# Optimization experiments

Measured on AMD Instinct MI355X. Metric: run time of the kernel, lower is better.

## Reference

```python
import jax, jax.numpy as jnp
import numpy as np

K = (0.3, 0.3, 0.4)   # args.args_k_0..2
EPS = 1e-8


def squash(v, axis=-1):
    norm = jnp.linalg.norm(v, axis=axis, keepdims=True)
    scale = norm ** 2 / (1.0 + norm ** 2) / (norm + EPS)
    return scale * v


def setup_inputs() -> dict:
    key = jax.random.key(0)
    kx, kw = jax.random.split(key)
    B, IN, DIN, OUT, DOUT = 128, 4608, 8, 10, 16
    x = jax.random.normal(kx, (B, IN, DIN), dtype=jnp.float32)
    weight = 0.1 * jax.random.normal(kw, (OUT, IN, DOUT, DIN), dtype=jnp.float32)
    return {"x": x, "weight": weight}


def reference(x, weight):
    # x: [B, I, Din], weight: [O, I, Dout, Din]
    # x_hat[b,o,i,d] = sum_k weight[o,i,d,k] * x[b,i,k]
    x_hat = jnp.einsum('oidk,bik->boid', weight, x)  # [B, O, I, Dout]
    x_hat_d = jax.lax.stop_gradient(x_hat)
    B, O, I, D = x_hat.shape
    b = jnp.zeros((B, O, I), dtype=x.dtype)
    feats = []
    for it in range(3):
        c = jax.nn.softmax(b, axis=1)[..., None]          # [B, O, I, 1], softmax over out caps
        if it == 2:
            out = squash(jnp.sum(c * x_hat, axis=-2, keepdims=True))      # [B, O, 1, D]
        else:
            out = squash(jnp.sum(c * x_hat_d, axis=-2, keepdims=True))    # [B, O, 1, D]
            b = b + jnp.sum(out * x_hat_d, axis=-1)                       # agreement update
        feats.append(out * K[it])
    # stack -> [3, B, O, 1, D]; squeeze caps-sum axis; sum over iterations
    outputs = jnp.sum(jnp.squeeze(jnp.stack(feats), axis=-2), axis=0)     # [B, O, D]
    return outputs.reshape(B, O, 4, 4)
```

## Files before the change

### kernel.cpp

```cpp
#include <hip/hip_runtime.h>

#define B_    128
#define I_    4608
#define O_    10
#define D_    16
#define NCHUNKS 2304
#define NIB   64
#define CPB   36
#define CHH   2560
#define PSET  20480

typedef _Float16 f16x2 __attribute__((ext_vector_type(2)));
typedef _Float16 f16x4 __attribute__((ext_vector_type(4)));
typedef _Float16 f16x8 __attribute__((ext_vector_type(8)));
typedef float    f32x4 __attribute__((ext_vector_type(4)));
typedef __fp16   pk16x2 __attribute__((ext_vector_type(2)));
typedef unsigned int uint2v __attribute__((ext_vector_type(2)));

__device__ __forceinline__ f16x4 pack4(float a, float b, float c, float d) {
    union { f16x4 v; pk16x2 p[2]; } u;
    u.p[0] = __builtin_amdgcn_cvt_pkrtz(a, b);
    u.p[1] = __builtin_amdgcn_cvt_pkrtz(c, d);
    return u.v;
}
__device__ __forceinline__ f16x2 splat_h2(float a) {
    union { f16x2 v; pk16x2 p; } u;
    u.p = __builtin_amdgcn_cvt_pkrtz(a, a);
    return u.v;
}

__global__ __launch_bounds__(256)
void prep_kernel(const float* __restrict__ w, _Float16* __restrict__ pw)
{
    __shared__ float wch[2560];
    const int c = blockIdx.x, t = threadIdx.x;
#pragma unroll
    for (int o = 0; o < O_; ++o)
        wch[o * 256 + t] = w[(long)o * (I_ * 128) + (long)c * 256 + t];
    __syncthreads();

    _Float16* dst = pw + (long)c * CHH;
#pragma unroll
    for (int kk = 0; kk < 3; ++kk) {
        const int sidx = t + kk * 256;
        if (sidx < 640) {
            const int hg   = sidx & 1;
            const int lane = (sidx >> 1) & 63;
            const int p    = sidx >> 7;
            const int r = lane & 15, g = lane >> 4;
            const int o = 2 * p + hg;
            const float4 gg = *(const float4*)&wch[o * 256 + (g & 1) * 128 + r * 8 + (g >> 1) * 4];
            *(f16x4*)(dst + (long)sidx * 4) = pack4(gg.x, gg.y, gg.z, gg.w);
        }
    }
}

template<int MODE>
__global__ __launch_bounds__(512, 4)
void pass_kernel(const float* __restrict__ x,
                 const _Float16* __restrict__ pw,
                 const float* __restrict__ v,
                 float* __restrict__ parts)
{
    __shared__ float red[4 * 2560];

    const int tid  = threadIdx.x;
    const int lane = tid & 63;
    const int wv   = tid >> 6;
    const int bl   = lane & 15;
    const int g    = lane >> 4;
    const int u    = blockIdx.x;
    const int xcd  = u & 7, s = u >> 3;
    const int ib   = xcd * 8 + (s & 7);
    const int bg   = s >> 3;
    const int c0   = ib * CPB;
    const int cend = c0 + CPB;
    const int iloc = g & 1, kq = g >> 1;
    const int b0   = bg * 16 + bl;

    f16x4 idf;
#pragma unroll
    for (int j = 0; j < 4; ++j) idf[j] = (_Float16)((bl == 4 * g + j) ? 1.f : 0.f);

    f16x4 vf[O_];
    if (MODE == 1) {
#pragma unroll
        for (int o = 0; o < O_; ++o) {
            const float4 vv = *(const float4*)(v + ((long)b0 * O_ + o) * D_ + g * 4);
            vf[o] = pack4(vv.x, vv.y, vv.z, vv.w);
        }
    }

    f32x4 S[O_];
#pragma unroll
    for (int o = 0; o < O_; ++o) S[o] = (f32x4)(0.f);

    const long lofs = (long)lane * 8;
    auto fragp = [&](int c, int p) {
        return (const f16x8*)(pw + (long)c * CHH + p * 512 + lofs);
    };
    auto xp = [&](int c) {
        return (const float4*)(x + ((long)b0 * I_ + 2 * c + iloc) * 8 + kq * 4);
    };

    int c = c0 + wv;
    f16x8 f1[5];
    float4 xqC, xqN;
#pragma unroll
    for (int p = 0; p < 5; ++p) f1[p] = *fragp(c, p);
    xqC = *xp(c);

#pragma unroll
    for (int t5 = 0; t5 < 5; ++t5) {
        const bool valid = (c < cend);
        int cn = c + 8; if (cn > NCHUNKS - 1) cn = NCHUNKS - 1;
        if (valid) {
            xqN = *xp(cn);

            float cs[O_];
            if (MODE == 1) {
#pragma unroll
                for (int p = 0; p < 5; ++p) {
                    f16x4 pe, po;
                    pe[0]=f1[p][0]; pe[1]=f1[p][1]; pe[2]=f1[p][2]; pe[3]=f1[p][3];
                    po[0]=f1[p][4]; po[1]=f1[p][5]; po[2]=f1[p][6]; po[3]=f1[p][7];
                    const f32x4 te = __builtin_amdgcn_mfma_f32_16x16x16f16(pe, idf, (f32x4)(0.f), 0, 0, 0);
                    const f32x4 to = __builtin_amdgcn_mfma_f32_16x16x16f16(po, idf, (f32x4)(0.f), 0, 0, 0);
                    const f16x4 ae = pack4(te[0], te[1], te[2], te[3]);
                    const f16x4 ao = pack4(to[0], to[1], to[2], to[3]);
                    const f32x4 ua = __builtin_amdgcn_mfma_f32_16x16x16f16(ae, vf[2*p],   (f32x4)(0.f), 0, 0, 0);
                    const f32x4 ub = __builtin_amdgcn_mfma_f32_16x16x16f16(ao, vf[2*p+1], (f32x4)(0.f), 0, 0, 0);
                    float d0 = ua[0] * xqC.x; d0 = fmaf(ua[1], xqC.y, d0);
                    d0 = fmaf(ua[2], xqC.z, d0); d0 = fmaf(ua[3], xqC.w, d0);
                    float d1 = ub[0] * xqC.x; d1 = fmaf(ub[1], xqC.y, d1);
                    d1 = fmaf(ub[2], xqC.z, d1); d1 = fmaf(ub[3], xqC.w, d1);
                    cs[2*p] = d0; cs[2*p+1] = d1;
                }
                float ssum = 0.f;
#pragma unroll
                for (int o = 0; o < O_; ++o) {
                    const unsigned int tt = __float_as_uint(cs[o]);
                    const uint2v sw = __builtin_amdgcn_permlane32_swap(tt, tt, false, false);
                    const float e = __expf(__uint_as_float(sw[0]) + __uint_as_float(sw[1]));
                    cs[o] = e; ssum += e;
                }
                const float inv = 1.f / ssum;
#pragma unroll
                for (int o = 0; o < O_; ++o) cs[o] *= inv;
            }

            union F4 { f16x4 v; f16x2 h[2]; };
            F4 xh;
            xh.v = pack4(xqC.x, xqC.y, xqC.z, xqC.w);
#pragma unroll
            for (int p = 0; p < 5; ++p) {
                f16x4 pe, po;
                pe[0]=f1[p][0]; pe[1]=f1[p][1]; pe[2]=f1[p][2]; pe[3]=f1[p][3];
                po[0]=f1[p][4]; po[1]=f1[p][5]; po[2]=f1[p][6]; po[3]=f1[p][7];
                F4 ye, yo;
                if (MODE == 0) { ye = xh; yo = xh; }
                else {
                    const f16x2 ce = splat_h2(cs[2*p]);
                    const f16x2 co = splat_h2(cs[2*p+1]);
                    ye.h[0] = xh.h[0] * ce; ye.h[1] = xh.h[1] * ce;
                    yo.h[0] = xh.h[0] * co; yo.h[1] = xh.h[1] * co;
                }
                S[2*p]   = __builtin_amdgcn_mfma_f32_16x16x16f16(pe, ye.v, S[2*p],   0, 0, 0);
                S[2*p+1] = __builtin_amdgcn_mfma_f32_16x16x16f16(po, yo.v, S[2*p+1], 0, 0, 0);
            }
#pragma unroll
            for (int p = 0; p < 5; ++p) f1[p] = *fragp(cn, p);
            xqC = xqN;
        }
        c += 8;
    }

    auto slot = [&](int w, int o) {
        return &red[w * 2560 + o * 256 + lane * 4];
    };
#define TREE_WR(WSRC)                                                       \
    if (wv >= WSRC && wv < 2 * WSRC) {                                      \
        _Pragma("unroll") for (int o = 0; o < O_; ++o)                      \
            *(f32x4*)slot(wv - WSRC, o) = S[o];                             \
    }                                                                       \
    __syncthreads();                                                        \
    if (wv < WSRC) {                                                        \
        _Pragma("unroll") for (int o = 0; o < O_; ++o)                      \
            S[o] += *(f32x4*)slot(wv, o);                                   \
    }                                                                       \
    __syncthreads();

    TREE_WR(4)
    TREE_WR(2)
    TREE_WR(1)
#undef TREE_WR

    if (wv == 0) {
#pragma unroll
        for (int o = 0; o < O_; ++o) {
            float* pp = parts + (long)ib * PSET + ((long)b0 * O_ + o) * D_ + g * 4;
            *(f32x4*)pp = S[o];
        }
    }
}

__global__ __launch_bounds__(256)
void reduce_squash(const float* __restrict__ parts, float* __restrict__ v_buf,
                   float* __restrict__ out, float kscale, float pre, int mode)
{
    __shared__ float red2[4][16];
    const int tid  = threadIdx.x;
    const int lane = tid & 63;
    const int wv   = tid >> 6;
    const int g2   = blockIdx.x;
    const int pg   = tid >> 4;
    const int d    = tid & 15;

    float s = 0.f;
#pragma unroll
    for (int k = 0; k < 4; ++k)
        s += parts[(long)(pg * 4 + k) * PSET + g2 * D_ + d];

    s += __shfl_xor(s, 16);
    s += __shfl_xor(s, 32);
    if (lane < 16) red2[wv][lane] = s;
    __syncthreads();

    if (tid < 16) {
        float tot = (red2[0][tid] + red2[1][tid]) + (red2[2][tid] + red2[3][tid]);
        tot *= pre;
        float n2 = tot * tot;
        n2 += __shfl_xor(n2, 1);
        n2 += __shfl_xor(n2, 2);
        n2 += __shfl_xor(n2, 4);
        n2 += __shfl_xor(n2, 8);
        const float n     = sqrtf(n2);
        const float scale = n2 / ((1.f + n2) * (n + 1e-8f));
        const float o_    = scale * tot;
        const int idx = g2 * D_ + tid;
        if (mode == 0)      { v_buf[idx] = o_;  out[idx]  = kscale * o_; }
        else if (mode == 1) { v_buf[idx] += o_; out[idx] += kscale * o_; }
        else                {                   out[idx] += kscale * o_; }
    }
}

extern "C" void kernel_launch(void* const* d_in, const int* in_sizes, int n_in,
                              void* d_out, int out_size, void* d_ws, size_t ws_size,
                              hipStream_t stream)
{
    const float* x = (const float*)d_in[0];
    const float* w = (const float*)d_in[1];
    float* out   = (float*)d_out;
    float* parts = (float*)d_ws;
    float* v_buf = parts + (long)NIB * PSET;
    _Float16* pw = (_Float16*)(v_buf + B_ * O_ * D_);

    prep_kernel<<<NCHUNKS, 256, 0, stream>>>(w, pw);

    pass_kernel<0><<<512, 512, 0, stream>>>(x, pw, v_buf, parts);
    reduce_squash<<<1280, 256, 0, stream>>>(parts, v_buf, out, 0.3f, 0.1f, 0);

    pass_kernel<1><<<512, 512, 0, stream>>>(x, pw, v_buf, parts);
    reduce_squash<<<1280, 256, 0, stream>>>(parts, v_buf, out, 0.3f, 1.0f, 1);

    pass_kernel<1><<<512, 512, 0, stream>>>(x, pw, v_buf, parts);
    reduce_squash<<<1280, 256, 0, stream>>>(parts, v_buf, out, 0.4f, 1.0f, 2);
}
```

Measured before the change: 66.53 us.

## Fuse reduce_squash into pass_kernel via last-blocks atomic counter

```diff
diff --git a/kernel.cpp b/kernel.cpp
--- a/kernel.cpp
+++ b/kernel.cpp
@@ -9,6 +9,8 @@
 #define CPB   36
 #define CHH   2560
 #define PSET  20480
+#define NB_   512
+#define NRED  160
 
 typedef _Float16 f16x2 __attribute__((ext_vector_type(2)));
 typedef _Float16 f16x4 __attribute__((ext_vector_type(4)));
@@ -30,10 +32,12 @@
 }
 
 __global__ __launch_bounds__(256)
-void prep_kernel(const float* __restrict__ w, _Float16* __restrict__ pw)
+void prep_kernel(const float* __restrict__ w, _Float16* __restrict__ pw,
+                 unsigned* __restrict__ cnt)
 {
     __shared__ float wch[2560];
     const int c = blockIdx.x, t = threadIdx.x;
+    if (c == 0 && t < 3) cnt[t] = 0u;
 #pragma unroll
     for (int o = 0; o < O_; ++o)
         wch[o * 256 + t] = w[(long)o * (I_ * 128) + (long)c * 256 + t];
@@ -60,9 +64,14 @@
 void pass_kernel(const float* __restrict__ x,
                  const _Float16* __restrict__ pw,
                  const float* __restrict__ v,
-                 float* __restrict__ parts)
+                 float* __restrict__ parts,
+                 float* __restrict__ v_buf,
+                 float* __restrict__ out,
+                 float kscale, float pre, int mode,
+                 unsigned* __restrict__ cnt)
 {
     __shared__ float red[4 * 2560];
+    __shared__ unsigned retS;
 
     const int tid  = threadIdx.x;
     const int lane = tid & 63;
@@ -202,45 +211,46 @@
             *(f32x4*)pp = S[o];
         }
     }
-}
-
-__global__ __launch_bounds__(256)
-void reduce_squash(const float* __restrict__ parts, float* __restrict__ v_buf,
-                   float* __restrict__ out, float kscale, float pre, int mode)
-{
-    __shared__ float red2[4][16];
-    const int tid  = threadIdx.x;
-    const int lane = tid & 63;
-    const int wv   = tid >> 6;
-    const int g2   = blockIdx.x;
-    const int pg   = tid >> 4;
-    const int d    = tid & 15;
-
-    float s = 0.f;
-#pragma unroll
-    for (int k = 0; k < 4; ++k)
-        s += parts[(long)(pg * 4 + k) * PSET + g2 * D_ + d];
-
-    s += __shfl_xor(s, 16);
-    s += __shfl_xor(s, 32);
-    if (lane < 16) red2[wv][lane] = s;
-    __syncthreads();
-
-    if (tid < 16) {
-        float tot = (red2[0][tid] + red2[1][tid]) + (red2[2][tid] + red2[3][tid]);
-        tot *= pre;
-        float n2 = tot * tot;
+
+    __syncthreads();
+    if (tid == 0) {
+        __threadfence();
+        const unsigned r = __hip_atomic_fetch_add(cnt, 1u, __ATOMIC_ACQ_REL,
+                                                  __HIP_MEMORY_SCOPE_AGENT);
+        retS = r;
+        if (r >= (unsigned)(NB_ - NRED)) {
+            while (__hip_atomic_load(cnt, __ATOMIC_ACQUIRE,
+                                     __HIP_MEMORY_SCOPE_AGENT) < (unsigned)NB_)
+                __builtin_amdgcn_s_sleep(2);
+        }
+    }
+    __syncthreads();
+    const unsigned r = retS;
+    if (r >= (unsigned)(NB_ - NRED)) {
+        __threadfence();
+        const int unit = ((int)r - (NB_ - NRED)) * 8 + wv;
+        const int pg = lane >> 4, d = lane & 15;
+        float sac = 0.f;
+#pragma unroll
+        for (int k = 0; k < 16; ++k)
+            sac += parts[(long)(pg * 16 + k) * PSET + unit * D_ + d];
+        sac += __shfl_xor(sac, 16);
+        sac += __shfl_xor(sac, 32);
+        sac *= pre;
+        float n2 = sac * sac;
         n2 += __shfl_xor(n2, 1);
         n2 += __shfl_xor(n2, 2);
         n2 += __shfl_xor(n2, 4);
         n2 += __shfl_xor(n2, 8);
-        const float n     = sqrtf(n2);
-        const float scale = n2 / ((1.f + n2) * (n + 1e-8f));
-        const float o_    = scale * tot;
-        const int idx = g2 * D_ + tid;
-        if (mode == 0)      { v_buf[idx] = o_;  out[idx]  = kscale * o_; }
-        else if (mode == 1) { v_buf[idx] += o_; out[idx] += kscale * o_; }
-        else                {                   out[idx] += kscale * o_; }
+        if (lane < 16) {
+            const float n     = sqrtf(n2);
+            const float scale = n2 / ((1.f + n2) * (n + 1e-8f));
+            const float o_    = scale * sac;
+            const int idx = unit * D_ + lane;
+            if (mode == 0)      { v_buf[idx] = o_;  out[idx]  = kscale * o_; }
+            else if (mode == 1) { v_buf[idx] += o_; out[idx] += kscale * o_; }
+            else                {                   out[idx] += kscale * o_; }
+        }
     }
 }
 
@@ -254,15 +264,14 @@
     float* parts = (float*)d_ws;
     float* v_buf = parts + (long)NIB * PSET;
     _Float16* pw = (_Float16*)(v_buf + B_ * O_ * D_);
-
-    prep_kernel<<<NCHUNKS, 256, 0, stream>>>(w, pw);
-
-    pass_kernel<0><<<512, 512, 0, stream>>>(x, pw, v_buf, parts);
-    reduce_squash<<<1280, 256, 0, stream>>>(parts, v_buf, out, 0.3f, 0.1f, 0);
-
-    pass_kernel<1><<<512, 512, 0, stream>>>(x, pw, v_buf, parts);
-    reduce_squash<<<1280, 256, 0, stream>>>(parts, v_buf, out, 0.3f, 1.0f, 1);
-
-    pass_kernel<1><<<512, 512, 0, stream>>>(x, pw, v_buf, parts);
-    reduce_squash<<<1280, 256, 0, stream>>>(parts, v_buf, out, 0.4f, 1.0f, 2);
-}
+    unsigned* cnt = (unsigned*)((char*)d_ws + (32l << 20));
+
+    prep_kernel<<<NCHUNKS, 256, 0, stream>>>(w, pw, cnt);
+
+    pass_kernel<0><<<NB_, 512, 0, stream>>>(x, pw, v_buf, parts, v_buf, out,
+                                            0.3f, 0.1f, 0, cnt + 0);
+    pass_kernel<1><<<NB_, 512, 0, stream>>>(x, pw, v_buf, parts, v_buf, out,
+                                            0.3f, 1.0f, 1, cnt + 1);
+    pass_kernel<1><<<NB_, 512, 0, stream>>>(x, pw, v_buf, parts, v_buf, out,
+                                            0.4f, 1.0f, 2, cnt + 2);
+}
```

Result: slower. 236.8 us (+256.0%).
